# Kernel optimization log

Hardware: AMD Instinct MI355X
Metric: run time of the kernel (lower is better)

Reference implementation:

```python
import jax, jax.numpy as jnp
import numpy as np

N_NODES = 10000
IN_CH = 128
HID = 256
OUT_CH = 1
N_EDGES_ADJ = 320000  # avg degree 32
N_TARGET = 8192


def setup_inputs() -> dict:
    key = jax.random.key(0)
    ks = jax.random.split(key, 16)
    s = 0.05  # weight scale for numerical stability
    inp = {
        'x': jax.random.normal(ks[0], (N_NODES, IN_CH), jnp.float32),
        'adj_row': jax.random.randint(ks[1], (N_EDGES_ADJ,), 0, N_NODES),
        'adj_col': jax.random.randint(ks[2], (N_EDGES_ADJ,), 0, N_NODES),
        'tar_ei': jax.random.randint(ks[3], (2, N_TARGET), 0, N_NODES),
        'beta': jnp.ones((1,), jnp.float32),
        'W1': s * jax.random.normal(ks[4], (IN_CH, HID), jnp.float32),
        'b1': jnp.zeros((HID,), jnp.float32),
        'W2': s * jax.random.normal(ks[5], (HID, HID), jnp.float32),
        'b2': jnp.zeros((HID,), jnp.float32),
        'W3': s * jax.random.normal(ks[6], (HID, HID), jnp.float32),
        'b3': jnp.zeros((HID,), jnp.float32),
        'Wij1': s * jax.random.normal(ks[7], (IN_CH, HID), jnp.float32),
        'bij1': jnp.zeros((HID,), jnp.float32),
        'Wij2': s * jax.random.normal(ks[8], (HID, HID), jnp.float32),
        'bij2': jnp.zeros((HID,), jnp.float32),
        'Wl1': s * jax.random.normal(ks[9], (HID, HID), jnp.float32),
        'bl1': jnp.zeros((HID,), jnp.float32),
        'Wl2': s * jax.random.normal(ks[10], (HID, OUT_CH), jnp.float32),
        'bl2': jnp.zeros((OUT_CH,), jnp.float32),
    }
    return inp


def reference(x, adj_row, adj_col, tar_ei, beta, W1, b1, W2, b2, W3, b3,
              Wij1, bij1, Wij2, bij2, Wl1, bl1, Wl2, bl2):
    n = x.shape[0]
    # Binary adjacency (duplicates collapse to 1, matching SparseTensor semantics)
    A = jnp.zeros((n, n), x.dtype).at[adj_row, adj_col].set(1.0)
    xi = x[tar_ei[0]]  # [E, F]
    xj = x[tar_ei[1]]  # [E, F]
    # adjoverlap: common-neighbor indicator per target edge, then spmm_add with x
    cn_mask = A[tar_ei[0]] * A[tar_ei[1]]          # [E, N]
    cn_x = cn_mask @ x                              # [E, F] sum of features over common neighbors
    # xcnlin: Linear-ReLU-Linear-ReLU-Linear (eval mode: dropout=identity, ln=identity)
    xcn = jax.nn.relu(cn_x @ W1 + b1)
    xcn = jax.nn.relu(xcn @ W2 + b2)
    xcn = xcn @ W3 + b3
    # xijlin: Linear-ReLU-Linear
    xij = jax.nn.relu((xi * xj) @ Wij1 + bij1) @ Wij2 + bij2
    # lin head: Linear-ReLU-Linear
    h = jax.nn.relu((xcn * beta + xij) @ Wl1 + bl1)
    return h @ Wl2 + bl2  # [E, 1]
```

## Files before the change

kernel.cpp:

```cpp
#include <hip/hip_runtime.h>
#include <hip/hip_bf16.h>

#define N_NODES 10000
#define IN_CH 128
#define HID 256
#define E_TAR 8192
#define N_EDGES 320000
#define WPR 320
#define WUSED 313
#define MASK_WORDS (N_NODES * WPR)
#define CSR_MAX 128
#define BM 32

typedef short bf16x8 __attribute__((ext_vector_type(8)));
typedef short bf16x4 __attribute__((ext_vector_type(4)));
typedef float f32x4 __attribute__((ext_vector_type(4)));

__device__ __forceinline__ unsigned short f2bf(float f) {
  union { float f; unsigned u; } v; v.f = f;
  unsigned r = v.u + 0x7fffu + ((v.u >> 16) & 1u);
  return (unsigned short)(r >> 16);
}
__device__ __forceinline__ float bf2f(unsigned short h) {
  union { unsigned u; float f; } v; v.u = ((unsigned)h) << 16; return v.f;
}

__global__ void prep_and_fill(const float* __restrict__ W1, const float* __restrict__ W2,
                              const float* __restrict__ W3, const float* __restrict__ Wij1,
                              const float* __restrict__ Wij2, const float* __restrict__ Wl1,
                              unsigned short* __restrict__ wts,
                              uint4* __restrict__ zbase, int n4) {
  if (blockIdx.x >= 320) {
    int i = (blockIdx.x - 320) * 256 + threadIdx.x;
    int stride = 3200 * 256;
    uint4 z = {0u, 0u, 0u, 0u};
    for (; i < n4; i += stride) zbase[i] = z;
    return;
  }
  int bid = blockIdx.x;
  const float* W; unsigned short* O; int K, t;
  if      (bid <  32) { W = W1;   O = wts;          K = 128; t = bid; }
  else if (bid <  96) { W = W2;   O = wts + 32768;  K = 256; t = bid - 32; }
  else if (bid < 160) { W = W3;   O = wts + 98304;  K = 256; t = bid - 96; }
  else if (bid < 192) { W = Wij1; O = wts + 163840; K = 128; t = bid - 160; }
  else if (bid < 256) { W = Wij2; O = wts + 196608; K = 256; t = bid - 192; }
  else                { W = Wl1;  O = wts + 262144; K = 256; t = bid - 256; }
  const int N = 256;
  int tpk = K / 32;
  int tk = t % tpk, tn = t / tpk;
  __shared__ float tile[32][33];
  int tid = threadIdx.x;
  int c = tid & 31, r0 = tid >> 5;
  #pragma unroll
  for (int rr = 0; rr < 32; rr += 8)
    tile[r0 + rr][c] = W[(size_t)(tk * 32 + r0 + rr) * N + tn * 32 + c];
  __syncthreads();
  #pragma unroll
  for (int rr = 0; rr < 32; rr += 8)
    O[(size_t)(tn * 32 + r0 + rr) * K + tk * 32 + c] = f2bf(tile[c][r0 + rr]);
}

__global__ void scatter_adj(const int* __restrict__ row, const int* __restrict__ col,
                            unsigned* __restrict__ mask, int* __restrict__ deg,
                            int* __restrict__ csr) {
  int k = blockIdx.x * 256 + threadIdx.x;
  if (k < N_EDGES) {
    int r = row[k], c = col[k];
    unsigned bit = 1u << (c & 31);
    unsigned old = atomicOr(&mask[(size_t)r * WPR + (c >> 5)], bit);
    if (!(old & bit)) {
      int p = atomicAdd(&deg[r], 1);
      if (p < CSR_MAX) csr[(size_t)r * CSR_MAX + p] = c;
    }
  }
}

template<int KN>
__device__ __forceinline__ void loadB(const unsigned short* __restrict__ Wt,
                                      int wn, int l15, int kg,
                                      bf16x8* b0, bf16x8* b1) {
  const unsigned short* p0 = Wt + (size_t)(wn + l15) * KN + kg;
  const unsigned short* p1 = Wt + (size_t)(wn + 16 + l15) * KN + kg;
  #pragma unroll
  for (int s = 0; s < KN / 32; ++s) {
    b0[s] = *(const bf16x8*)(p0 + s * 32);
    b1[s] = *(const bf16x8*)(p1 + s * 32);
  }
}

template<int K>
__device__ __forceinline__ void computeL(const unsigned short (*A)[264],
                                         const bf16x8* b0, const bf16x8* b1,
                                         int l15, int kg, f32x4 acc[2][2]) {
  #pragma unroll
  for (int s = 0; s < K / 32; ++s) {
    bf16x8 a0 = *(const bf16x8*)&A[l15][s * 32 + kg];
    bf16x8 a1 = *(const bf16x8*)&A[16 + l15][s * 32 + kg];
    acc[0][0] = __builtin_amdgcn_mfma_f32_16x16x32_bf16(a0, b0[s], acc[0][0], 0, 0, 0);
    acc[1][0] = __builtin_amdgcn_mfma_f32_16x16x32_bf16(a1, b0[s], acc[1][0], 0, 0, 0);
    acc[0][1] = __builtin_amdgcn_mfma_f32_16x16x32_bf16(a0, b1[s], acc[0][1], 0, 0, 0);
    acc[1][1] = __builtin_amdgcn_mfma_f32_16x16x32_bf16(a1, b1[s], acc[1][1], 0, 0, 0);
  }
}

__global__ __launch_bounds__(512, 2) void fused_all(
    const unsigned* __restrict__ mask, const int* __restrict__ deg,
    const int* __restrict__ csr, const int* __restrict__ tar,
    const float* __restrict__ x, const unsigned short* __restrict__ wts,
    const float* __restrict__ b1, const float* __restrict__ b2, const float* __restrict__ b3,
    const float* __restrict__ bij1, const float* __restrict__ bij2, const float* __restrict__ bl1,
    const float* __restrict__ Wl2, const float* __restrict__ bl2,
    const float* __restrict__ betaPtr, float* __restrict__ out)
{
  __shared__ unsigned short P[BM][264];
  __shared__ unsigned short Q[BM][264];
  const unsigned short* Wt1   = wts;
  const unsigned short* Wt2   = wts + 32768;
  const unsigned short* Wt3   = wts + 98304;
  const unsigned short* Wtij1 = wts + 163840;
  const unsigned short* Wtij2 = wts + 196608;
  const unsigned short* Wtl1  = wts + 262144;

  int m0 = blockIdx.x * BM;
  int tid = threadIdx.x;
  int lane = tid & 63, wv = tid >> 6;
  int wn = wv * 32;
  int l15 = lane & 15, kg = (lane >> 4) * 8, rq = (lane >> 4) * 4;

  bf16x8 B0[8], B1[8];
  loadB<128>(Wt1, wn, l15, kg, B0, B1);

  int row = tid >> 4, seg = tid & 15;
  int gi = tar[m0 + row], gj = tar[E_TAR + m0 + row];
  const float* xip = x + (size_t)gi * IN_CH + seg * 8;
  const float* xjp = x + (size_t)gj * IN_CH + seg * 8;
  f32x4 xi0 = *(const f32x4*)xip, xi1 = *(const f32x4*)(xip + 4);
  f32x4 xj0 = *(const f32x4*)xjp, xj1 = *(const f32x4*)(xjp + 4);
  float bv1[2]   = { b1[wn + l15],   b1[wn + 16 + l15] };
  float bv2[2]   = { b2[wn + l15],   b2[wn + 16 + l15] };
  float bv3[2]   = { b3[wn + l15],   b3[wn + 16 + l15] };
  float bvij1[2] = { bij1[wn + l15], bij1[wn + 16 + l15] };
  float bvij2[2] = { bij2[wn + l15], bij2[wn + 16 + l15] };
  float bvl1[2]  = { bl1[wn + l15],  bl1[wn + 16 + l15] };
  float beta_v = betaPtr[0];
  f32x4 w2v = *(const f32x4*)&Wl2[lane * 4];

  float g0[4] = {0.f, 0.f, 0.f, 0.f}, g1[4] = {0.f, 0.f, 0.f, 0.f};
  #pragma unroll
  for (int q = 0; q < 4; ++q) {
    int e  = m0 + wv * 4 + q;
    int ti = tar[e], tj = tar[E_TAR + e];
    int di = deg[ti], dj = deg[tj];
    int a  = (di <= dj) ? ti : tj;
    int b  = (di <= dj) ? tj : ti;
    int da = min(di, dj);
    const unsigned* mb = mask + (size_t)b * WPR;
    const int* la = csr + (size_t)a * CSR_MAX;
    int nit = (da + 63) >> 6;
    for (int it = 0; it < nit; ++it) {
      int t = it * 64 + lane;
      int n = 0; bool hit = false;
      if (t < da) {
        n = la[t];
        hit = (mb[n >> 5] >> (n & 31)) & 1u;
      }
      unsigned long long bal = __ballot(hit);
      while (bal) {
        int src = __ffsll((unsigned long long)bal) - 1;
        bal &= bal - 1;
        int nb = __shfl(n, src);
        const float* xr = x + (size_t)nb * IN_CH;
        g0[q] += xr[lane];
        g1[q] += xr[lane + 64];
      }
    }
  }
  #pragma unroll
  for (int q = 0; q < 4; ++q) {
    int r = wv * 4 + q;
    P[r][lane]      = f2bf(g0[q]);
    P[r][64 + lane] = f2bf(g1[q]);
  }
  __syncthreads();

  f32x4 acc[2][2];
  #define ZACC { acc[0][0]=(f32x4){0,0,0,0}; acc[0][1]=(f32x4){0,0,0,0}; \
                 acc[1][0]=(f32x4){0,0,0,0}; acc[1][1]=(f32x4){0,0,0,0}; }
  #define EPI(dst, bv, RELU) { \
    _Pragma("unroll") for (int nf = 0; nf < 2; ++nf) { \
      int cg = wn + nf * 16 + l15; \
      _Pragma("unroll") for (int m = 0; m < 2; ++m) \
        _Pragma("unroll") for (int i = 0; i < 4; ++i) { \
          float v = acc[m][nf][i] + bv[nf]; \
          if (RELU) v = fmaxf(v, 0.f); \
          dst[m * 16 + rq + i][cg] = f2bf(v); \
        } \
    } }

  ZACC; computeL<128>(P, B0, B1, l15, kg, acc);
  loadB<256>(Wt2, wn, l15, kg, B0, B1);
  EPI(Q, bv1, 1);
  __syncthreads();

  ZACC; computeL<256>(Q, B0, B1, l15, kg, acc);
  loadB<256>(Wt3, wn, l15, kg, B0, B1);
  EPI(P, bv2, 1);
  __syncthreads();

  f32x4 xcn[2][2];
  xcn[0][0]=(f32x4){0,0,0,0}; xcn[0][1]=(f32x4){0,0,0,0};
  xcn[1][0]=(f32x4){0,0,0,0}; xcn[1][1]=(f32x4){0,0,0,0};
  computeL<256>(P, B0, B1, l15, kg, xcn);
  loadB<128>(Wtij1, wn, l15, kg, B0, B1);
  #pragma unroll
  for (int nf = 0; nf < 2; ++nf)
    #pragma unroll
    for (int m = 0; m < 2; ++m)
      #pragma unroll
      for (int i = 0; i < 4; ++i) xcn[m][nf][i] += bv3[nf];
  __syncthreads();

  {
    unsigned short tmp[8];
    #pragma unroll
    for (int u = 0; u < 4; ++u) {
      tmp[u] = f2bf(xi0[u] * xj0[u]);
      tmp[4 + u] = f2bf(xi1[u] * xj1[u]);
    }
    *(bf16x8*)&P[row][seg * 8] = *(bf16x8*)tmp;
  }
  __syncthreads();

  ZACC; computeL<128>(P, B0, B1, l15, kg, acc);
  loadB<256>(Wtij2, wn, l15, kg, B0, B1);
  EPI(Q, bvij1, 1);
  __syncthreads();

  ZACC; computeL<256>(Q, B0, B1, l15, kg, acc);
  loadB<256>(Wtl1, wn, l15, kg, B0, B1);
  #pragma unroll
  for (int nf = 0; nf < 2; ++nf) {
    int cg = wn + nf * 16 + l15;
    #pragma unroll
    for (int m = 0; m < 2; ++m)
      #pragma unroll
      for (int i = 0; i < 4; ++i) {
        float v = acc[m][nf][i] + bvij2[nf] + beta_v * xcn[m][nf][i];
        P[m * 16 + rq + i][cg] = f2bf(v);
      }
  }
  __syncthreads();

  ZACC; computeL<256>(P, B0, B1, l15, kg, acc);
  EPI(Q, bvl1, 1);
  __syncthreads();

  {
    float bl2v = bl2[0];
    #pragma unroll
    for (int rr = 0; rr < 4; ++rr) {
      int r = wv * 4 + rr;
      bf16x4 q = *(const bf16x4*)&Q[r][lane * 4];
      float s = 0.f;
      #pragma unroll
      for (int u = 0; u < 4; ++u) s += bf2f((unsigned short)q[u]) * w2v[u];
      #pragma unroll
      for (int off = 32; off; off >>= 1) s += __shfl_down(s, off);
      if (lane == 0) out[m0 + r] = s + bl2v;
    }
  }
}

extern "C" void kernel_launch(void* const* d_in, const int* in_sizes, int n_in,
                              void* d_out, int out_size, void* d_ws, size_t ws_size,
                              hipStream_t stream) {
  const float* x      = (const float*)d_in[0];
  const int*   adj_r  = (const int*)d_in[1];
  const int*   adj_c  = (const int*)d_in[2];
  const int*   tar    = (const int*)d_in[3];
  const float* beta   = (const float*)d_in[4];
  const float* W1     = (const float*)d_in[5];
  const float* b1     = (const float*)d_in[6];
  const float* W2     = (const float*)d_in[7];
  const float* b2     = (const float*)d_in[8];
  const float* W3     = (const float*)d_in[9];
  const float* b3     = (const float*)d_in[10];
  const float* Wij1   = (const float*)d_in[11];
  const float* bij1   = (const float*)d_in[12];
  const float* Wij2   = (const float*)d_in[13];
  const float* bij2   = (const float*)d_in[14];
  const float* Wl1    = (const float*)d_in[15];
  const float* bl1    = (const float*)d_in[16];
  const float* Wl2    = (const float*)d_in[17];
  const float* bl2    = (const float*)d_in[18];

  char* ws = (char*)d_ws;
  unsigned*       mask = (unsigned*)ws;
  int*            deg  = (int*)(ws + (size_t)MASK_WORDS * 4);
  int*            csr  = (int*)(ws + (size_t)15 * 1024 * 1024);
  unsigned short* wts  = (unsigned short*)(ws + (size_t)21 * 1024 * 1024);

  prep_and_fill<<<3520, 256, 0, stream>>>(W1, W2, W3, Wij1, Wij2, Wl1, wts,
                                          (uint4*)mask, (MASK_WORDS + N_NODES) / 4);
  scatter_adj<<<(N_EDGES + 255) / 256, 256, 0, stream>>>(adj_r, adj_c, mask, deg, csr);
  fused_all<<<E_TAR / BM, 512, 0, stream>>>(mask, deg, csr, tar, x, wts,
                                            b1, b2, b3, bij1, bij2, bl1,
                                            Wl2, bl2, beta, (float*)d_out);
}
```

Measured before the change: 72.71 us.

## Merge three kernels into one cooperative kernel with grid-wide syncs

Merges mask zeroing and weight transpose, the adjacency scatter, and the fused MLP pipeline into a single cooperative launch of 256 blocks. Two grid.sync barriers separate the phases, which removes the separate kernel launches and their gaps. In exchange the zero-fill and scatter phases now run on only 256 blocks instead of thousands. Grid-wide barriers also add their own cost.

```diff
diff --git a/kernel.cpp b/kernel.cpp
--- a/kernel.cpp
+++ b/kernel.cpp
@@ -1,5 +1,8 @@
 #include <hip/hip_runtime.h>
+#include <hip/hip_cooperative_groups.h>
 #include <hip/hip_bf16.h>
+
+namespace cg = cooperative_groups;
 
 #define N_NODES 10000
 #define IN_CH 128
@@ -7,10 +10,11 @@
 #define E_TAR 8192
 #define N_EDGES 320000
 #define WPR 320
-#define WUSED 313
 #define MASK_WORDS (N_NODES * WPR)
 #define CSR_MAX 128
 #define BM 32
+#define GRID 256
+#define TPB 512
 
 typedef short bf16x8 __attribute__((ext_vector_type(8)));
 typedef short bf16x4 __attribute__((ext_vector_type(4)));
@@ -25,55 +29,14 @@
   union { unsigned u; float f; } v; v.u = ((unsigned)h) << 16; return v.f;
 }
 
-__global__ void prep_and_fill(const float* __restrict__ W1, const float* __restrict__ W2,
-                              const float* __restrict__ W3, const float* __restrict__ Wij1,
-                              const float* __restrict__ Wij2, const float* __restrict__ Wl1,
-                              unsigned short* __restrict__ wts,
-                              uint4* __restrict__ zbase, int n4) {
-  if (blockIdx.x >= 320) {
-    int i = (blockIdx.x - 320) * 256 + threadIdx.x;
-    int stride = 3200 * 256;
-    uint4 z = {0u, 0u, 0u, 0u};
-    for (; i < n4; i += stride) zbase[i] = z;
-    return;
-  }
-  int bid = blockIdx.x;
-  const float* W; unsigned short* O; int K, t;
-  if      (bid <  32) { W = W1;   O = wts;          K = 128; t = bid; }
-  else if (bid <  96) { W = W2;   O = wts + 32768;  K = 256; t = bid - 32; }
-  else if (bid < 160) { W = W3;   O = wts + 98304;  K = 256; t = bid - 96; }
-  else if (bid < 192) { W = Wij1; O = wts + 163840; K = 128; t = bid - 160; }
-  else if (bid < 256) { W = Wij2; O = wts + 196608; K = 256; t = bid - 192; }
-  else                { W = Wl1;  O = wts + 262144; K = 256; t = bid - 256; }
-  const int N = 256;
-  int tpk = K / 32;
-  int tk = t % tpk, tn = t / tpk;
-  __shared__ float tile[32][33];
-  int tid = threadIdx.x;
-  int c = tid & 31, r0 = tid >> 5;
-  #pragma unroll
-  for (int rr = 0; rr < 32; rr += 8)
-    tile[r0 + rr][c] = W[(size_t)(tk * 32 + r0 + rr) * N + tn * 32 + c];
-  __syncthreads();
-  #pragma unroll
-  for (int rr = 0; rr < 32; rr += 8)
-    O[(size_t)(tn * 32 + r0 + rr) * K + tk * 32 + c] = f2bf(tile[c][r0 + rr]);
-}
-
-__global__ void scatter_adj(const int* __restrict__ row, const int* __restrict__ col,
-                            unsigned* __restrict__ mask, int* __restrict__ deg,
-                            int* __restrict__ csr) {
-  int k = blockIdx.x * 256 + threadIdx.x;
-  if (k < N_EDGES) {
-    int r = row[k], c = col[k];
-    unsigned bit = 1u << (c & 31);
-    unsigned old = atomicOr(&mask[(size_t)r * WPR + (c >> 5)], bit);
-    if (!(old & bit)) {
-      int p = atomicAdd(&deg[r], 1);
-      if (p < CSR_MAX) csr[(size_t)r * CSR_MAX + p] = c;
-    }
-  }
-}
+struct KParams {
+  const float* x; const int* tar; const int* adj_r; const int* adj_c;
+  const float* beta;
+  const float *W1, *b1, *W2, *b2, *W3, *b3;
+  const float *Wij1, *bij1, *Wij2, *bij2, *Wl1, *bl1, *Wl2, *bl2;
+  unsigned* mask; int* deg; int* csr; unsigned short* wts;
+  float* out;
+};
 
 template<int KN>
 __device__ __forceinline__ void loadB(const unsigned short* __restrict__ Wt,
@@ -103,59 +66,89 @@
   }
 }
 
-__global__ __launch_bounds__(512, 2) void fused_all(
-    const unsigned* __restrict__ mask, const int* __restrict__ deg,
-    const int* __restrict__ csr, const int* __restrict__ tar,
-    const float* __restrict__ x, const unsigned short* __restrict__ wts,
-    const float* __restrict__ b1, const float* __restrict__ b2, const float* __restrict__ b3,
-    const float* __restrict__ bij1, const float* __restrict__ bij2, const float* __restrict__ bl1,
-    const float* __restrict__ Wl2, const float* __restrict__ bl2,
-    const float* __restrict__ betaPtr, float* __restrict__ out)
-{
+__global__ __launch_bounds__(TPB, 2) void fused_pipeline(KParams p) {
   __shared__ unsigned short P[BM][264];
   __shared__ unsigned short Q[BM][264];
-  const unsigned short* Wt1   = wts;
-  const unsigned short* Wt2   = wts + 32768;
-  const unsigned short* Wt3   = wts + 98304;
-  const unsigned short* Wtij1 = wts + 163840;
-  const unsigned short* Wtij2 = wts + 196608;
-  const unsigned short* Wtl1  = wts + 262144;
-
-  int m0 = blockIdx.x * BM;
+  __shared__ float tile[32][33];
+  cg::grid_group grid = cg::this_grid();
+
   int tid = threadIdx.x;
   int lane = tid & 63, wv = tid >> 6;
   int wn = wv * 32;
   int l15 = lane & 15, kg = (lane >> 4) * 8, rq = (lane >> 4) * 4;
-
-  bf16x8 B0[8], B1[8];
-  loadB<128>(Wt1, wn, l15, kg, B0, B1);
+  int m0 = blockIdx.x * BM;
 
   int row = tid >> 4, seg = tid & 15;
-  int gi = tar[m0 + row], gj = tar[E_TAR + m0 + row];
-  const float* xip = x + (size_t)gi * IN_CH + seg * 8;
-  const float* xjp = x + (size_t)gj * IN_CH + seg * 8;
+  int gi = p.tar[m0 + row], gj = p.tar[E_TAR + m0 + row];
+  const float* xip = p.x + (size_t)gi * IN_CH + seg * 8;
+  const float* xjp = p.x + (size_t)gj * IN_CH + seg * 8;
   f32x4 xi0 = *(const f32x4*)xip, xi1 = *(const f32x4*)(xip + 4);
   f32x4 xj0 = *(const f32x4*)xjp, xj1 = *(const f32x4*)(xjp + 4);
-  float bv1[2]   = { b1[wn + l15],   b1[wn + 16 + l15] };
-  float bv2[2]   = { b2[wn + l15],   b2[wn + 16 + l15] };
-  float bv3[2]   = { b3[wn + l15],   b3[wn + 16 + l15] };
-  float bvij1[2] = { bij1[wn + l15], bij1[wn + 16 + l15] };
-  float bvij2[2] = { bij2[wn + l15], bij2[wn + 16 + l15] };
-  float bvl1[2]  = { bl1[wn + l15],  bl1[wn + 16 + l15] };
-  float beta_v = betaPtr[0];
-  f32x4 w2v = *(const f32x4*)&Wl2[lane * 4];
+  float bv1[2]   = { p.b1[wn + l15],   p.b1[wn + 16 + l15] };
+  float bv2[2]   = { p.b2[wn + l15],   p.b2[wn + 16 + l15] };
+  float bv3[2]   = { p.b3[wn + l15],   p.b3[wn + 16 + l15] };
+  float bvij1[2] = { p.bij1[wn + l15], p.bij1[wn + 16 + l15] };
+  float bvij2[2] = { p.bij2[wn + l15], p.bij2[wn + 16 + l15] };
+  float bvl1[2]  = { p.bl1[wn + l15],  p.bl1[wn + 16 + l15] };
+  float beta_v = p.beta[0];
+  f32x4 w2v = *(const f32x4*)&p.Wl2[lane * 4];
+
+  {
+    uint4 z = {0u, 0u, 0u, 0u};
+    uint4* zp = (uint4*)p.mask;
+    const int n4 = (MASK_WORDS + N_NODES) / 4;
+    for (int i = blockIdx.x * TPB + tid; i < n4; i += GRID * TPB) zp[i] = z;
+  }
+  for (int t0 = blockIdx.x; t0 < 320; t0 += GRID) {
+    const float* W; unsigned short* O; int K, t;
+    if      (t0 <  32) { W = p.W1;   O = p.wts;          K = 128; t = t0; }
+    else if (t0 <  96) { W = p.W2;   O = p.wts + 32768;  K = 256; t = t0 - 32; }
+    else if (t0 < 160) { W = p.W3;   O = p.wts + 98304;  K = 256; t = t0 - 96; }
+    else if (t0 < 192) { W = p.Wij1; O = p.wts + 163840; K = 128; t = t0 - 160; }
+    else if (t0 < 256) { W = p.Wij2; O = p.wts + 196608; K = 256; t = t0 - 192; }
+    else               { W = p.Wl1;  O = p.wts + 262144; K = 256; t = t0 - 256; }
+    int tpk = K / 32, tk = t % tpk, tn = t / tpk;
+    int c = tid & 31, r = tid >> 5;
+    __syncthreads();
+    tile[r][c]      = W[(size_t)(tk * 32 + r) * 256 + tn * 32 + c];
+    tile[r + 16][c] = W[(size_t)(tk * 32 + r + 16) * 256 + tn * 32 + c];
+    __syncthreads();
+    O[(size_t)(tn * 32 + r) * K + tk * 32 + c]      = f2bf(tile[c][r]);
+    O[(size_t)(tn * 32 + r + 16) * K + tk * 32 + c] = f2bf(tile[c][r + 16]);
+  }
+  grid.sync();
+
+  for (int k = blockIdx.x * TPB + tid; k < N_EDGES; k += GRID * TPB) {
+    int r = p.adj_r[k], c = p.adj_c[k];
+    unsigned bit = 1u << (c & 31);
+    unsigned old = atomicOr(&p.mask[(size_t)r * WPR + (c >> 5)], bit);
+    if (!(old & bit)) {
+      int q = atomicAdd(&p.deg[r], 1);
+      if (q < CSR_MAX) p.csr[(size_t)r * CSR_MAX + q] = c;
+    }
+  }
+  grid.sync();
+
+  bf16x8 B0[8], B1[8];
+  loadB<128>(p.wts, wn, l15, kg, B0, B1);
+
+  int ti[4], tj[4], di[4], dj[4];
+  #pragma unroll
+  for (int q = 0; q < 4; ++q) {
+    int e = m0 + wv * 4 + q;
+    ti[q] = p.tar[e]; tj[q] = p.tar[E_TAR + e];
+  }
+  #pragma unroll
+  for (int q = 0; q < 4; ++q) { di[q] = p.deg[ti[q]]; dj[q] = p.deg[tj[q]]; }
 
   float g0[4] = {0.f, 0.f, 0.f, 0.f}, g1[4] = {0.f, 0.f, 0.f, 0.f};
   #pragma unroll
   for (int q = 0; q < 4; ++q) {
-    int e  = m0 + wv * 4 + q;
-    int ti = tar[e], tj = tar[E_TAR + e];
-    int di = deg[ti], dj = deg[tj];
-    int a  = (di <= dj) ? ti : tj;
-    int b  = (di <= dj) ? tj : ti;
-    int da = min(di, dj);
-    const unsigned* mb = mask + (size_t)b * WPR;
-    const int* la = csr + (size_t)a * CSR_MAX;
+    int a  = (di[q] <= dj[q]) ? ti[q] : tj[q];
+    int b  = (di[q] <= dj[q]) ? tj[q] : ti[q];
+    int da = min(di[q], dj[q]);
+    const unsigned* mb = p.mask + (size_t)b * WPR;
+    const int* la = p.csr + (size_t)a * CSR_MAX;
     int nit = (da + 63) >> 6;
     for (int it = 0; it < nit; ++it) {
       int t = it * 64 + lane;
@@ -166,15 +159,16 @@
       }
       unsigned long long bal = __ballot(hit);
       while (bal) {
-        int src = __ffsll((unsigned long long)bal) - 1;
+        int src = __ffsll(bal) - 1;
         bal &= bal - 1;
         int nb = __shfl(n, src);
-        const float* xr = x + (size_t)nb * IN_CH;
+        const float* xr = p.x + (size_t)nb * IN_CH;
         g0[q] += xr[lane];
         g1[q] += xr[lane + 64];
       }
     }
   }
+  __syncthreads();
   #pragma unroll
   for (int q = 0; q < 4; ++q) {
     int r = wv * 4 + q;
@@ -198,12 +192,12 @@
     } }
 
   ZACC; computeL<128>(P, B0, B1, l15, kg, acc);
-  loadB<256>(Wt2, wn, l15, kg, B0, B1);
+  loadB<256>(p.wts + 32768, wn, l15, kg, B0, B1);
   EPI(Q, bv1, 1);
   __syncthreads();
 
   ZACC; computeL<256>(Q, B0, B1, l15, kg, acc);
-  loadB<256>(Wt3, wn, l15, kg, B0, B1);
+  loadB<256>(p.wts + 98304, wn, l15, kg, B0, B1);
   EPI(P, bv2, 1);
   __syncthreads();
 
@@ -211,7 +205,7 @@
   xcn[0][0]=(f32x4){0,0,0,0}; xcn[0][1]=(f32x4){0,0,0,0};
   xcn[1][0]=(f32x4){0,0,0,0}; xcn[1][1]=(f32x4){0,0,0,0};
   computeL<256>(P, B0, B1, l15, kg, xcn);
-  loadB<128>(Wtij1, wn, l15, kg, B0, B1);
+  loadB<128>(p.wts + 163840, wn, l15, kg, B0, B1);
   #pragma unroll
   for (int nf = 0; nf < 2; ++nf)
     #pragma unroll
@@ -232,12 +226,12 @@
   __syncthreads();
 
   ZACC; computeL<128>(P, B0, B1, l15, kg, acc);
-  loadB<256>(Wtij2, wn, l15, kg, B0, B1);
+  loadB<256>(p.wts + 196608, wn, l15, kg, B0, B1);
   EPI(Q, bvij1, 1);
   __syncthreads();
 
   ZACC; computeL<256>(Q, B0, B1, l15, kg, acc);
-  loadB<256>(Wtl1, wn, l15, kg, B0, B1);
+  loadB<256>(p.wts + 262144, wn, l15, kg, B0, B1);
   #pragma unroll
   for (int nf = 0; nf < 2; ++nf) {
     int cg = wn + nf * 16 + l15;
@@ -256,7 +250,7 @@
   __syncthreads();
 
   {
-    float bl2v = bl2[0];
+    float bl2v = p.bl2[0];
     #pragma unroll
     for (int rr = 0; rr < 4; ++rr) {
       int r = wv * 4 + rr;
@@ -266,7 +260,7 @@
       for (int u = 0; u < 4; ++u) s += bf2f((unsigned short)q[u]) * w2v[u];
       #pragma unroll
       for (int off = 32; off; off >>= 1) s += __shfl_down(s, off);
-      if (lane == 0) out[m0 + r] = s + bl2v;
+      if (lane == 0) p.out[m0 + r] = s + bl2v;
     }
   }
 }
@@ -274,36 +268,27 @@
 extern "C" void kernel_launch(void* const* d_in, const int* in_sizes, int n_in,
                               void* d_out, int out_size, void* d_ws, size_t ws_size,
                               hipStream_t stream) {
-  const float* x      = (const float*)d_in[0];
-  const int*   adj_r  = (const int*)d_in[1];
-  const int*   adj_c  = (const int*)d_in[2];
-  const int*   tar    = (const int*)d_in[3];
-  const float* beta   = (const float*)d_in[4];
-  const float* W1     = (const float*)d_in[5];
-  const float* b1     = (const float*)d_in[6];
-  const float* W2     = (const float*)d_in[7];
-  const float* b2     = (const float*)d_in[8];
-  const float* W3     = (const float*)d_in[9];
-  const float* b3     = (const float*)d_in[10];
-  const float* Wij1   = (const float*)d_in[11];
-  const float* bij1   = (const float*)d_in[12];
-  const float* Wij2   = (const float*)d_in[13];
-  const float* bij2   = (const float*)d_in[14];
-  const float* Wl1    = (const float*)d_in[15];
-  const float* bl1    = (const float*)d_in[16];
-  const float* Wl2    = (const float*)d_in[17];
-  const float* bl2    = (const float*)d_in[18];
-
   char* ws = (char*)d_ws;
-  unsigned*       mask = (unsigned*)ws;
-  int*            deg  = (int*)(ws + (size_t)MASK_WORDS * 4);
-  int*            csr  = (int*)(ws + (size_t)15 * 1024 * 1024);
-  unsigned short* wts  = (unsigned short*)(ws + (size_t)21 * 1024 * 1024);
-
-  prep_and_fill<<<3520, 256, 0, stream>>>(W1, W2, W3, Wij1, Wij2, Wl1, wts,
-                                          (uint4*)mask, (MASK_WORDS + N_NODES) / 4);
-  scatter_adj<<<(N_EDGES + 255) / 256, 256, 0, stream>>>(adj_r, adj_c, mask, deg, csr);
-  fused_all<<<E_TAR / BM, 512, 0, stream>>>(mask, deg, csr, tar, x, wts,
-                                            b1, b2, b3, bij1, bij2, bl1,
-                                            Wl2, bl2, beta, (float*)d_out);
-}
+  KParams prm;
+  prm.x     = (const float*)d_in[0];
+  prm.adj_r = (const int*)d_in[1];
+  prm.adj_c = (const int*)d_in[2];
+  prm.tar   = (const int*)d_in[3];
+  prm.beta  = (const float*)d_in[4];
+  prm.W1    = (const float*)d_in[5];  prm.b1   = (const float*)d_in[6];
+  prm.W2    = (const float*)d_in[7];  prm.b2   = (const float*)d_in[8];
+  prm.W3    = (const float*)d_in[9];  prm.b3   = (const float*)d_in[10];
+  prm.Wij1  = (const float*)d_in[11]; prm.bij1 = (const float*)d_in[12];
+  prm.Wij2  = (const float*)d_in[13]; prm.bij2 = (const float*)d_in[14];
+  prm.Wl1   = (const float*)d_in[15]; prm.bl1  = (const float*)d_in[16];
+  prm.Wl2   = (const float*)d_in[17]; prm.bl2  = (const float*)d_in[18];
+  prm.mask  = (unsigned*)ws;
+  prm.deg   = (int*)(ws + (size_t)MASK_WORDS * 4);
+  prm.csr   = (int*)(ws + (size_t)15 * 1024 * 1024);
+  prm.wts   = (unsigned short*)(ws + (size_t)21 * 1024 * 1024);
+  prm.out   = (float*)d_out;
+
+  void* args[] = { &prm };
+  hipLaunchCooperativeKernel((const void*)fused_pipeline, dim3(GRID), dim3(TPB),
+                             args, 0, stream);
+}
```

Result: slower. 143.1 us (+96.8%).

## Replace dense bitmask adjacency with CSR list intersection and in-wave dedup

Applied to the files above, without the earlier changes.

Drops the 12.8 MB dense adjacency bitmask, along with its zero-fill and atomicOr scatter. Common neighbors are now found by intersecting the two targets' CSR lists with wave shuffles, and duplicate edges are removed by an O(d^2) scan within the shorter list. The goal is to cut the memory-fill and atomic traffic, paid for with more compute in the fused kernel. The GEMM helpers are also rewritten as macros over named registers, and degrees are clamped to CSR_MAX.

```diff
diff --git a/kernel.cpp b/kernel.cpp
--- a/kernel.cpp
+++ b/kernel.cpp
@@ -6,9 +6,6 @@
 #define HID 256
 #define E_TAR 8192
 #define N_EDGES 320000
-#define WPR 320
-#define WUSED 313
-#define MASK_WORDS (N_NODES * WPR)
 #define CSR_MAX 128
 #define BM 32
 
@@ -25,16 +22,13 @@
   union { unsigned u; float f; } v; v.u = ((unsigned)h) << 16; return v.f;
 }
 
-__global__ void prep_and_fill(const float* __restrict__ W1, const float* __restrict__ W2,
-                              const float* __restrict__ W3, const float* __restrict__ Wij1,
-                              const float* __restrict__ Wij2, const float* __restrict__ Wl1,
-                              unsigned short* __restrict__ wts,
-                              uint4* __restrict__ zbase, int n4) {
+__global__ void prep_w(const float* __restrict__ W1, const float* __restrict__ W2,
+                       const float* __restrict__ W3, const float* __restrict__ Wij1,
+                       const float* __restrict__ Wij2, const float* __restrict__ Wl1,
+                       unsigned short* __restrict__ wts, uint4* __restrict__ degz) {
   if (blockIdx.x >= 320) {
     int i = (blockIdx.x - 320) * 256 + threadIdx.x;
-    int stride = 3200 * 256;
-    uint4 z = {0u, 0u, 0u, 0u};
-    for (; i < n4; i += stride) zbase[i] = z;
+    if (i < (N_NODES + 3) / 4) degz[i] = (uint4){0u, 0u, 0u, 0u};
     return;
   }
   int bid = blockIdx.x;
@@ -45,68 +39,33 @@
   else if (bid < 192) { W = Wij1; O = wts + 163840; K = 128; t = bid - 160; }
   else if (bid < 256) { W = Wij2; O = wts + 196608; K = 256; t = bid - 192; }
   else                { W = Wl1;  O = wts + 262144; K = 256; t = bid - 256; }
-  const int N = 256;
-  int tpk = K / 32;
-  int tk = t % tpk, tn = t / tpk;
+  int tpk = K / 32, tk = t % tpk, tn = t / tpk;
   __shared__ float tile[32][33];
   int tid = threadIdx.x;
   int c = tid & 31, r0 = tid >> 5;
   #pragma unroll
   for (int rr = 0; rr < 32; rr += 8)
-    tile[r0 + rr][c] = W[(size_t)(tk * 32 + r0 + rr) * N + tn * 32 + c];
+    tile[r0 + rr][c] = W[(size_t)(tk * 32 + r0 + rr) * 256 + tn * 32 + c];
   __syncthreads();
   #pragma unroll
   for (int rr = 0; rr < 32; rr += 8)
     O[(size_t)(tn * 32 + r0 + rr) * K + tk * 32 + c] = f2bf(tile[c][r0 + rr]);
 }
 
-__global__ void scatter_adj(const int* __restrict__ row, const int* __restrict__ col,
-                            unsigned* __restrict__ mask, int* __restrict__ deg,
-                            int* __restrict__ csr) {
+__global__ void scatter_csr(const int* __restrict__ row, const int* __restrict__ col,
+                            int* __restrict__ deg, int* __restrict__ csr) {
   int k = blockIdx.x * 256 + threadIdx.x;
   if (k < N_EDGES) {
     int r = row[k], c = col[k];
-    unsigned bit = 1u << (c & 31);
-    unsigned old = atomicOr(&mask[(size_t)r * WPR + (c >> 5)], bit);
-    if (!(old & bit)) {
-      int p = atomicAdd(&deg[r], 1);
-      if (p < CSR_MAX) csr[(size_t)r * CSR_MAX + p] = c;
-    }
-  }
-}
-
-template<int KN>
-__device__ __forceinline__ void loadB(const unsigned short* __restrict__ Wt,
-                                      int wn, int l15, int kg,
-                                      bf16x8* b0, bf16x8* b1) {
-  const unsigned short* p0 = Wt + (size_t)(wn + l15) * KN + kg;
-  const unsigned short* p1 = Wt + (size_t)(wn + 16 + l15) * KN + kg;
-  #pragma unroll
-  for (int s = 0; s < KN / 32; ++s) {
-    b0[s] = *(const bf16x8*)(p0 + s * 32);
-    b1[s] = *(const bf16x8*)(p1 + s * 32);
-  }
-}
-
-template<int K>
-__device__ __forceinline__ void computeL(const unsigned short (*A)[264],
-                                         const bf16x8* b0, const bf16x8* b1,
-                                         int l15, int kg, f32x4 acc[2][2]) {
-  #pragma unroll
-  for (int s = 0; s < K / 32; ++s) {
-    bf16x8 a0 = *(const bf16x8*)&A[l15][s * 32 + kg];
-    bf16x8 a1 = *(const bf16x8*)&A[16 + l15][s * 32 + kg];
-    acc[0][0] = __builtin_amdgcn_mfma_f32_16x16x32_bf16(a0, b0[s], acc[0][0], 0, 0, 0);
-    acc[1][0] = __builtin_amdgcn_mfma_f32_16x16x32_bf16(a1, b0[s], acc[1][0], 0, 0, 0);
-    acc[0][1] = __builtin_amdgcn_mfma_f32_16x16x32_bf16(a0, b1[s], acc[0][1], 0, 0, 0);
-    acc[1][1] = __builtin_amdgcn_mfma_f32_16x16x32_bf16(a1, b1[s], acc[1][1], 0, 0, 0);
+    int p = atomicAdd(&deg[r], 1);
+    if (p < CSR_MAX) csr[(size_t)r * CSR_MAX + p] = c;
   }
 }
 
 __global__ __launch_bounds__(512, 2) void fused_all(
-    const unsigned* __restrict__ mask, const int* __restrict__ deg,
-    const int* __restrict__ csr, const int* __restrict__ tar,
-    const float* __restrict__ x, const unsigned short* __restrict__ wts,
+    const int* __restrict__ deg, const int* __restrict__ csr,
+    const int* __restrict__ tar, const float* __restrict__ x,
+    const unsigned short* __restrict__ wts,
     const float* __restrict__ b1, const float* __restrict__ b2, const float* __restrict__ b3,
     const float* __restrict__ bij1, const float* __restrict__ bij2, const float* __restrict__ bl1,
     const float* __restrict__ Wl2, const float* __restrict__ bl2,
@@ -114,12 +73,6 @@
 {
   __shared__ unsigned short P[BM][264];
   __shared__ unsigned short Q[BM][264];
-  const unsigned short* Wt1   = wts;
-  const unsigned short* Wt2   = wts + 32768;
-  const unsigned short* Wt3   = wts + 98304;
-  const unsigned short* Wtij1 = wts + 163840;
-  const unsigned short* Wtij2 = wts + 196608;
-  const unsigned short* Wtl1  = wts + 262144;
 
   int m0 = blockIdx.x * BM;
   int tid = threadIdx.x;
@@ -127,8 +80,57 @@
   int wn = wv * 32;
   int l15 = lane & 15, kg = (lane >> 4) * 8, rq = (lane >> 4) * 4;
 
-  bf16x8 B0[8], B1[8];
-  loadB<128>(Wt1, wn, l15, kg, B0, B1);
+  bf16x8 Bv0, Bv1, Bv2, Bv3, Bv4, Bv5, Bv6, Bv7;
+  bf16x8 Bv8, Bv9, Bv10, Bv11, Bv12, Bv13, Bv14, Bv15;
+  f32x4 a00, a01, a10, a11;
+  f32x4 x00, x01, x10, x11;
+
+#define LB128(WT) { \
+    const unsigned short* _p = (WT) + (size_t)(wn + l15) * 128 + kg; \
+    const unsigned short* _q = (WT) + (size_t)(wn + 16 + l15) * 128 + kg; \
+    Bv0 = *(const bf16x8*)_p;        Bv1 = *(const bf16x8*)(_p + 32); \
+    Bv2 = *(const bf16x8*)(_p + 64); Bv3 = *(const bf16x8*)(_p + 96); \
+    Bv8 = *(const bf16x8*)_q;        Bv9 = *(const bf16x8*)(_q + 32); \
+    Bv10 = *(const bf16x8*)(_q + 64); Bv11 = *(const bf16x8*)(_q + 96); }
+
+#define LB256(WT) { \
+    const unsigned short* _p = (WT) + (size_t)(wn + l15) * 256 + kg; \
+    const unsigned short* _q = (WT) + (size_t)(wn + 16 + l15) * 256 + kg; \
+    Bv0 = *(const bf16x8*)_p;         Bv1 = *(const bf16x8*)(_p + 32); \
+    Bv2 = *(const bf16x8*)(_p + 64);  Bv3 = *(const bf16x8*)(_p + 96); \
+    Bv4 = *(const bf16x8*)(_p + 128); Bv5 = *(const bf16x8*)(_p + 160); \
+    Bv6 = *(const bf16x8*)(_p + 192); Bv7 = *(const bf16x8*)(_p + 224); \
+    Bv8 = *(const bf16x8*)_q;         Bv9 = *(const bf16x8*)(_q + 32); \
+    Bv10 = *(const bf16x8*)(_q + 64); Bv11 = *(const bf16x8*)(_q + 96); \
+    Bv12 = *(const bf16x8*)(_q + 128); Bv13 = *(const bf16x8*)(_q + 160); \
+    Bv14 = *(const bf16x8*)(_q + 192); Bv15 = *(const bf16x8*)(_q + 224); }
+
+#define ST(S, S8, AA) { \
+    bf16x8 _a0 = *(const bf16x8*)&AA[l15][S * 32 + kg]; \
+    bf16x8 _a1 = *(const bf16x8*)&AA[16 + l15][S * 32 + kg]; \
+    a00 = __builtin_amdgcn_mfma_f32_16x16x32_bf16(_a0, Bv##S,  a00, 0, 0, 0); \
+    a10 = __builtin_amdgcn_mfma_f32_16x16x32_bf16(_a1, Bv##S,  a10, 0, 0, 0); \
+    a01 = __builtin_amdgcn_mfma_f32_16x16x32_bf16(_a0, Bv##S8, a01, 0, 0, 0); \
+    a11 = __builtin_amdgcn_mfma_f32_16x16x32_bf16(_a1, Bv##S8, a11, 0, 0, 0); }
+
+#define CL128(AA) ST(0, 8, AA) ST(1, 9, AA) ST(2, 10, AA) ST(3, 11, AA)
+#define CL256(AA) CL128(AA) ST(4, 12, AA) ST(5, 13, AA) ST(6, 14, AA) ST(7, 15, AA)
+
+#define ZA { a00 = (f32x4){0,0,0,0}; a01 = (f32x4){0,0,0,0}; \
+             a10 = (f32x4){0,0,0,0}; a11 = (f32x4){0,0,0,0}; }
+
+#define EPIW(DST, BS0, BS1, RELU) { \
+    _Pragma("unroll") for (int i = 0; i < 4; ++i) { \
+      float v0 = a00[i] + BS0, v1 = a10[i] + BS0; \
+      float v2 = a01[i] + BS1, v3 = a11[i] + BS1; \
+      if (RELU) { v0 = fmaxf(v0, 0.f); v1 = fmaxf(v1, 0.f); \
+                  v2 = fmaxf(v2, 0.f); v3 = fmaxf(v3, 0.f); } \
+      DST[rq + i][wn + l15]           = f2bf(v0); \
+      DST[16 + rq + i][wn + l15]      = f2bf(v1); \
+      DST[rq + i][wn + 16 + l15]      = f2bf(v2); \
+      DST[16 + rq + i][wn + 16 + l15] = f2bf(v3); } }
+
+  LB128(wts);
 
   int row = tid >> 4, seg = tid & 15;
   int gi = tar[m0 + row], gj = tar[E_TAR + m0 + row];
@@ -136,39 +138,55 @@
   const float* xjp = x + (size_t)gj * IN_CH + seg * 8;
   f32x4 xi0 = *(const f32x4*)xip, xi1 = *(const f32x4*)(xip + 4);
   f32x4 xj0 = *(const f32x4*)xjp, xj1 = *(const f32x4*)(xjp + 4);
-  float bv1[2]   = { b1[wn + l15],   b1[wn + 16 + l15] };
-  float bv2[2]   = { b2[wn + l15],   b2[wn + 16 + l15] };
-  float bv3[2]   = { b3[wn + l15],   b3[wn + 16 + l15] };
-  float bvij1[2] = { bij1[wn + l15], bij1[wn + 16 + l15] };
-  float bvij2[2] = { bij2[wn + l15], bij2[wn + 16 + l15] };
-  float bvl1[2]  = { bl1[wn + l15],  bl1[wn + 16 + l15] };
+  float bv1_0   = b1[wn + l15],   bv1_1   = b1[wn + 16 + l15];
+  float bv2_0   = b2[wn + l15],   bv2_1   = b2[wn + 16 + l15];
+  float bv3_0   = b3[wn + l15],   bv3_1   = b3[wn + 16 + l15];
+  float bvij1_0 = bij1[wn + l15], bvij1_1 = bij1[wn + 16 + l15];
+  float bvij2_0 = bij2[wn + l15], bvij2_1 = bij2[wn + 16 + l15];
+  float bvl1_0  = bl1[wn + l15],  bvl1_1  = bl1[wn + 16 + l15];
   float beta_v = betaPtr[0];
   f32x4 w2v = *(const f32x4*)&Wl2[lane * 4];
 
   float g0[4] = {0.f, 0.f, 0.f, 0.f}, g1[4] = {0.f, 0.f, 0.f, 0.f};
   #pragma unroll
   for (int q = 0; q < 4; ++q) {
-    int e  = m0 + wv * 4 + q;
-    int ti = tar[e], tj = tar[E_TAR + e];
-    int di = deg[ti], dj = deg[tj];
-    int a  = (di <= dj) ? ti : tj;
-    int b  = (di <= dj) ? tj : ti;
-    int da = min(di, dj);
-    const unsigned* mb = mask + (size_t)b * WPR;
-    const int* la = csr + (size_t)a * CSR_MAX;
-    int nit = (da + 63) >> 6;
-    for (int it = 0; it < nit; ++it) {
-      int t = it * 64 + lane;
-      int n = 0; bool hit = false;
-      if (t < da) {
-        n = la[t];
-        hit = (mb[n >> 5] >> (n & 31)) & 1u;
+    int e = m0 + wv * 4 + q;
+    int ti_ = tar[e], tj_ = tar[E_TAR + e];
+    int di_ = min(deg[ti_], CSR_MAX), dj_ = min(deg[tj_], CSR_MAX);
+    int a_ = (di_ <= dj_) ? ti_ : tj_;
+    int b_ = (di_ <= dj_) ? tj_ : ti_;
+    int da_ = min(di_, dj_), db_ = max(di_, dj_);
+    const int* la = csr + (size_t)a_ * CSR_MAX;
+    const int* lb = csr + (size_t)b_ * CSR_MAX;
+    for (int ab = 0; ab < da_; ab += 64) {
+      int t = ab + lane;
+      int at = (t < da_) ? la[t] : -1;
+      bool hit = false;
+      for (int bb = 0; bb < db_; bb += 64) {
+        int u = bb + lane;
+        int bl = (u < db_) ? lb[u] : -2;
+        int lim = db_ - bb; if (lim > 64) lim = 64;
+        for (int j = 0; j < lim; ++j) {
+          int bj = __shfl(bl, j);
+          hit |= (at == bj);
+        }
       }
-      unsigned long long bal = __ballot(hit);
+      bool dup = false;
+      for (int pb = 0; pb <= ab; pb += 64) {
+        int u = pb + lane;
+        int av = (u < da_) ? la[u] : -3;
+        int lim = da_ - pb; if (lim > 64) lim = 64;
+        for (int k2 = 0; k2 < lim; ++k2) {
+          int ak = __shfl(av, k2);
+          dup |= ((pb + k2) < t && ak == at);
+        }
+      }
+      bool good = (t < da_) && hit && !dup;
+      unsigned long long bal = __ballot(good);
       while (bal) {
-        int src = __ffsll((unsigned long long)bal) - 1;
+        int src = __ffsll(bal) - 1;
         bal &= bal - 1;
-        int nb = __shfl(n, src);
+        int nb = __shfl(at, src);
         const float* xr = x + (size_t)nb * IN_CH;
         g0[q] += xr[lane];
         g1[q] += xr[lane + 64];
@@ -183,76 +201,49 @@
   }
   __syncthreads();
 
-  f32x4 acc[2][2];
-  #define ZACC { acc[0][0]=(f32x4){0,0,0,0}; acc[0][1]=(f32x4){0,0,0,0}; \
-                 acc[1][0]=(f32x4){0,0,0,0}; acc[1][1]=(f32x4){0,0,0,0}; }
-  #define EPI(dst, bv, RELU) { \
-    _Pragma("unroll") for (int nf = 0; nf < 2; ++nf) { \
-      int cg = wn + nf * 16 + l15; \
-      _Pragma("unroll") for (int m = 0; m < 2; ++m) \
-        _Pragma("unroll") for (int i = 0; i < 4; ++i) { \
-          float v = acc[m][nf][i] + bv[nf]; \
-          if (RELU) v = fmaxf(v, 0.f); \
-          dst[m * 16 + rq + i][cg] = f2bf(v); \
-        } \
-    } }
-
-  ZACC; computeL<128>(P, B0, B1, l15, kg, acc);
-  loadB<256>(Wt2, wn, l15, kg, B0, B1);
-  EPI(Q, bv1, 1);
-  __syncthreads();
-
-  ZACC; computeL<256>(Q, B0, B1, l15, kg, acc);
-  loadB<256>(Wt3, wn, l15, kg, B0, B1);
-  EPI(P, bv2, 1);
-  __syncthreads();
-
-  f32x4 xcn[2][2];
-  xcn[0][0]=(f32x4){0,0,0,0}; xcn[0][1]=(f32x4){0,0,0,0};
-  xcn[1][0]=(f32x4){0,0,0,0}; xcn[1][1]=(f32x4){0,0,0,0};
-  computeL<256>(P, B0, B1, l15, kg, xcn);
-  loadB<128>(Wtij1, wn, l15, kg, B0, B1);
-  #pragma unroll
-  for (int nf = 0; nf < 2; ++nf)
-    #pragma unroll
-    for (int m = 0; m < 2; ++m)
-      #pragma unroll
-      for (int i = 0; i < 4; ++i) xcn[m][nf][i] += bv3[nf];
+  ZA; CL128(P); LB256(wts + 32768); EPIW(Q, bv1_0, bv1_1, true);
+  __syncthreads();
+
+  ZA; CL256(Q); LB256(wts + 98304); EPIW(P, bv2_0, bv2_1, true);
+  __syncthreads();
+
+  ZA; CL256(P); LB128(wts + 163840);
+  #pragma unroll
+  for (int i = 0; i < 4; ++i) {
+    x00[i] = a00[i] + bv3_0; x10[i] = a10[i] + bv3_0;
+    x01[i] = a01[i] + bv3_1; x11[i] = a11[i] + bv3_1;
+  }
   __syncthreads();
 
   {
     unsigned short tmp[8];
     #pragma unroll
     for (int u = 0; u < 4; ++u) {
-      tmp[u] = f2bf(xi0[u] * xj0[u]);
+      tmp[u]     = f2bf(xi0[u] * xj0[u]);
       tmp[4 + u] = f2bf(xi1[u] * xj1[u]);
     }
     *(bf16x8*)&P[row][seg * 8] = *(bf16x8*)tmp;
   }
   __syncthreads();
 
-  ZACC; computeL<128>(P, B0, B1, l15, kg, acc);
-  loadB<256>(Wtij2, wn, l15, kg, B0, B1);
-  EPI(Q, bvij1, 1);
-  __syncthreads();
-
-  ZACC; computeL<256>(Q, B0, B1, l15, kg, acc);
-  loadB<256>(Wtl1, wn, l15, kg, B0, B1);
-  #pragma unroll
-  for (int nf = 0; nf < 2; ++nf) {
-    int cg = wn + nf * 16 + l15;
-    #pragma unroll
-    for (int m = 0; m < 2; ++m)
-      #pragma unroll
-      for (int i = 0; i < 4; ++i) {
-        float v = acc[m][nf][i] + bvij2[nf] + beta_v * xcn[m][nf][i];
-        P[m * 16 + rq + i][cg] = f2bf(v);
-      }
-  }
-  __syncthreads();
-
-  ZACC; computeL<256>(P, B0, B1, l15, kg, acc);
-  EPI(Q, bvl1, 1);
+  ZA; CL128(P); LB256(wts + 196608); EPIW(Q, bvij1_0, bvij1_1, true);
+  __syncthreads();
+
+  ZA; CL256(Q); LB256(wts + 262144);
+  #pragma unroll
+  for (int i = 0; i < 4; ++i) {
+    float v0 = a00[i] + bvij2_0 + beta_v * x00[i];
+    float v1 = a10[i] + bvij2_0 + beta_v * x10[i];
+    float v2 = a01[i] + bvij2_1 + beta_v * x01[i];
+    float v3 = a11[i] + bvij2_1 + beta_v * x11[i];
+    P[rq + i][wn + l15]           = f2bf(v0);
+    P[16 + rq + i][wn + l15]      = f2bf(v1);
+    P[rq + i][wn + 16 + l15]      = f2bf(v2);
+    P[16 + rq + i][wn + 16 + l15] = f2bf(v3);
+  }
+  __syncthreads();
+
+  ZA; CL256(P); EPIW(Q, bvl1_0, bvl1_1, true);
   __syncthreads();
 
   {
@@ -260,10 +251,10 @@
     #pragma unroll
     for (int rr = 0; rr < 4; ++rr) {
       int r = wv * 4 + rr;
-      bf16x4 q = *(const bf16x4*)&Q[r][lane * 4];
+      bf16x4 qv = *(const bf16x4*)&Q[r][lane * 4];
       float s = 0.f;
       #pragma unroll
-      for (int u = 0; u < 4; ++u) s += bf2f((unsigned short)q[u]) * w2v[u];
+      for (int u = 0; u < 4; ++u) s += bf2f((unsigned short)qv[u]) * w2v[u];
       #pragma unroll
       for (int off = 32; off; off >>= 1) s += __shfl_down(s, off);
       if (lane == 0) out[m0 + r] = s + bl2v;
@@ -295,15 +286,13 @@
   const float* bl2    = (const float*)d_in[18];
 
   char* ws = (char*)d_ws;
-  unsigned*       mask = (unsigned*)ws;
-  int*            deg  = (int*)(ws + (size_t)MASK_WORDS * 4);
-  int*            csr  = (int*)(ws + (size_t)15 * 1024 * 1024);
-  unsigned short* wts  = (unsigned short*)(ws + (size_t)21 * 1024 * 1024);
-
-  prep_and_fill<<<3520, 256, 0, stream>>>(W1, W2, W3, Wij1, Wij2, Wl1, wts,
-                                          (uint4*)mask, (MASK_WORDS + N_NODES) / 4);
-  scatter_adj<<<(N_EDGES + 255) / 256, 256, 0, stream>>>(adj_r, adj_c, mask, deg, csr);
-  fused_all<<<E_TAR / BM, 512, 0, stream>>>(mask, deg, csr, tar, x, wts,
+  int*            deg = (int*)ws;
+  int*            csr = (int*)(ws + (size_t)1 * 1024 * 1024);
+  unsigned short* wts = (unsigned short*)(ws + (size_t)8 * 1024 * 1024);
+
+  prep_w<<<330, 256, 0, stream>>>(W1, W2, W3, Wij1, Wij2, Wl1, wts, (uint4*)deg);
+  scatter_csr<<<(N_EDGES + 255) / 256, 256, 0, stream>>>(adj_r, adj_c, deg, csr);
+  fused_all<<<E_TAR / BM, 512, 0, stream>>>(deg, csr, tar, x, wts,
                                             b1, b2, b3, bij1, bij2, bl1,
                                             Wl2, bl2, beta, (float*)d_out);
 }
```

New measurement: 75.26 us. +3.5%, slower.
